# Kernel tuning notes

Measured on AMD Instinct MI355X. Metric: run time of the kernel, lower is better.

The kernel has to match this reference:

```python
import jax, jax.numpy as jnp
import numpy as np

B, N, D, L = 32, 1000, 256, 3


def setup_inputs() -> dict:
    key = jax.random.key(0)
    k1, k2, k3, k4 = jax.random.split(key, 4)
    x = jax.random.normal(k1, (B, N, D), dtype=jnp.float32)
    node_feature = jax.random.normal(k2, (B, N, D), dtype=jnp.float32)
    # GCNConv weights (PyG Linear, glorot) and biases, stacked over layers
    scale = jnp.sqrt(6.0 / (D + D)).astype(jnp.float32)
    Ws = jax.random.uniform(k3, (L, D, D), minval=-1.0, maxval=1.0, dtype=jnp.float32) * scale
    bs = jnp.zeros((L, D), dtype=jnp.float32)
    return {"x": x, "node_feature": node_feature, "Ws": Ws, "bs": bs}


def _gcn_norm_adj(n):
    # self_loop=False -> adjacency is all-ones (diagonal included), so
    # add_remaining_self_loops is a no-op; deg = n for every node.
    adj = jnp.ones((n, n), dtype=jnp.float32)
    deg = adj.sum(axis=1)
    dinv = jax.lax.rsqrt(deg)
    return dinv[:, None] * adj * dinv[None, :]  # == ones/n


def reference(x, node_feature, Ws, bs):
    # x is unused by the math (only its size is inspected in the original).
    A_norm = _gcn_norm_adj(node_feature.shape[1])
    h = node_feature
    for l in range(L):
        h = jnp.einsum('bnd,de->bne', h, Ws[l])          # linear transform
        h = jnp.einsum('mn,bnd->bmd', A_norm, h) + bs[l]  # normalized aggregation + bias
        if l < L - 1:
            h = jax.nn.relu(h)  # dropout is identity in eval mode
    update_node_feature = h + node_feature  # residual (unconditional in source)
    return (update_node_feature, node_feature)
```

## Files before the change

kernel.cpp:

```cpp
#include <hip/hip_runtime.h>

#define BB 32
#define NN 1000
#define DD 256
#define SS 25
#define RPS 40
#define ELEMS (BB * NN * DD)

__global__ __launch_bounds__(256) void k_colsum(const float* __restrict__ nf,
                                                float* __restrict__ partial) {
    const int s = blockIdx.x, b = blockIdx.y, t = threadIdx.x;
    const int rg = t >> 6, dg = t & 63;
    const float4* src = (const float4*)nf;
    float4 acc = make_float4(0.f, 0.f, 0.f, 0.f);
#pragma unroll
    for (int c = 0; c < RPS / 4; c++) {
        const int n = s * RPS + c * 4 + rg;
        float4 v = src[(b * NN + n) * (DD / 4) + dg];
        acc.x += v.x; acc.y += v.y; acc.z += v.z; acc.w += v.w;
    }
    __shared__ float red[1024];
    ((float4*)red)[rg * 64 + dg] = acc;
    __syncthreads();
    float sum = 0.f;
#pragma unroll
    for (int r = 0; r < 4; r++) sum += red[r * 256 + t];
    partial[(s * BB + b) * DD + t] = sum;
}

__global__ __launch_bounds__(256) void k_mlp(const float* __restrict__ partial,
                                             const float* __restrict__ Ws,
                                             const float* __restrict__ bsv,
                                             float* __restrict__ hrow) {
    const int b = blockIdx.x, t = threadIdx.x;
    __shared__ float h[DD];
    float sum = 0.f;
#pragma unroll 5
    for (int s = 0; s < SS; s++) sum += partial[(s * BB + b) * DD + t];
    h[t] = sum * (1.0f / (float)NN);
    __syncthreads();
    for (int l = 0; l < 3; l++) {
        const float* W = Ws + l * DD * DD;
        float acc = 0.f;
#pragma unroll 8
        for (int k4 = 0; k4 < DD / 4; k4++) {
            const float4 hv = ((const float4*)h)[k4];
            const int k = k4 * 4;
            acc += hv.x * W[(k + 0) * DD + t];
            acc += hv.y * W[(k + 1) * DD + t];
            acc += hv.z * W[(k + 2) * DD + t];
            acc += hv.w * W[(k + 3) * DD + t];
        }
        float o = acc + bsv[l * DD + t];
        if (l < 2) o = fmaxf(o, 0.f);
        __syncthreads();
        h[t] = o;
        __syncthreads();
    }
    hrow[b * DD + t] = h[t];
}

__global__ __launch_bounds__(256) void k_out(const float* __restrict__ nf,
                                             const float* __restrict__ hrow,
                                             float* __restrict__ out) {
    const int i = blockIdx.x * 256 + threadIdx.x;
    const int e = i * 4;
    const int b = e / (NN * DD);
    const int d0 = e & (DD - 1);
    float4 v = ((const float4*)nf)[i];
    float4 hv = *(const float4*)(hrow + b * DD + d0);
    float4 o = make_float4(v.x + hv.x, v.y + hv.y, v.z + hv.z, v.w + hv.w);
    ((float4*)out)[i] = o;
    ((float4*)(out + ELEMS))[i] = v;
}

extern "C" void kernel_launch(void* const* d_in, const int* in_sizes, int n_in,
                              void* d_out, int out_size, void* d_ws, size_t ws_size,
                              hipStream_t stream) {
    const float* nf  = (const float*)d_in[1];
    const float* Ws  = (const float*)d_in[2];
    const float* bsv = (const float*)d_in[3];
    float* out = (float*)d_out;

    float* partial = (float*)d_ws;
    float* hrow    = partial + SS * BB * DD;

    k_colsum<<<dim3(SS, BB), 256, 0, stream>>>(nf, partial);
    k_mlp<<<BB, 256, 0, stream>>>(partial, Ws, bsv, hrow);
    k_out<<<(ELEMS / 4) / 256, 256, 0, stream>>>(nf, hrow, out);
}
```

Baseline: 137.2 us.

## Fuse passthrough copy into column-sum pass and MLP into output pass

Replaces the three kernels with two. The first pass reads node features once, writes the passthrough copy and computes per-slice column sums. The second pass has each of 256 blocks recompute its batch's three-layer MLP on the mean and then write the residual output for its slice. This removes one launch and the hrow round trip, and the copy no longer needs its own read. The cost is 8x redundant MLP compute and only 256 blocks for the streaming passes, which may underfill the GPU.

```diff
diff --git a/kernel.cpp b/kernel.cpp
--- a/kernel.cpp
+++ b/kernel.cpp
@@ -3,41 +3,47 @@
 #define BB 32
 #define NN 1000
 #define DD 256
-#define SS 25
-#define RPS 40
 #define ELEMS (BB * NN * DD)
+#define SLICES 8
+#define ROWS 125
+#define F4S (ROWS * DD / 4)
 
-__global__ __launch_bounds__(256) void k_colsum(const float* __restrict__ nf,
-                                                float* __restrict__ partial) {
-    const int s = blockIdx.x, b = blockIdx.y, t = threadIdx.x;
-    const int rg = t >> 6, dg = t & 63;
+__global__ __launch_bounds__(256) void k_stage(const float* __restrict__ nf,
+                                               float* __restrict__ out1,
+                                               float* __restrict__ partial) {
+    const int j = blockIdx.x, t = threadIdx.x;
+    const int b = j >> 3, s = j & 7;
+    const int base = (b * NN + s * ROWS) * (DD / 4);
     const float4* src = (const float4*)nf;
+    float4* dst = (float4*)out1;
     float4 acc = make_float4(0.f, 0.f, 0.f, 0.f);
-#pragma unroll
-    for (int c = 0; c < RPS / 4; c++) {
-        const int n = s * RPS + c * 4 + rg;
-        float4 v = src[(b * NN + n) * (DD / 4) + dg];
+#pragma unroll 4
+    for (int idx = t; idx < F4S; idx += 256) {
+        float4 v = src[base + idx];
+        dst[base + idx] = v;
         acc.x += v.x; acc.y += v.y; acc.z += v.z; acc.w += v.w;
     }
     __shared__ float red[1024];
-    ((float4*)red)[rg * 64 + dg] = acc;
+    ((float4*)red)[(t >> 6) * 64 + (t & 63)] = acc;
     __syncthreads();
     float sum = 0.f;
 #pragma unroll
     for (int r = 0; r < 4; r++) sum += red[r * 256 + t];
-    partial[(s * BB + b) * DD + t] = sum;
+    partial[j * DD + t] = sum;
 }
 
-__global__ __launch_bounds__(256) void k_mlp(const float* __restrict__ partial,
-                                             const float* __restrict__ Ws,
-                                             const float* __restrict__ bsv,
-                                             float* __restrict__ hrow) {
-    const int b = blockIdx.x, t = threadIdx.x;
+__global__ __launch_bounds__(256) void k_mlp_out(const float* __restrict__ nf,
+                                                 const float* __restrict__ partial,
+                                                 const float* __restrict__ Ws,
+                                                 const float* __restrict__ bsv,
+                                                 float* __restrict__ out0) {
+    const int j = blockIdx.x, t = threadIdx.x;
+    const int b = j >> 3, s = j & 7;
     __shared__ float h[DD];
-    float sum = 0.f;
-#pragma unroll 5
-    for (int s = 0; s < SS; s++) sum += partial[(s * BB + b) * DD + t];
-    h[t] = sum * (1.0f / (float)NN);
+    float m = 0.f;
+#pragma unroll
+    for (int i = 0; i < SLICES; i++) m += partial[(b * SLICES + i) * DD + t];
+    h[t] = m * (1.0f / (float)NN);
     __syncthreads();
     for (int l = 0; l < 3; l++) {
         const float* W = Ws + l * DD * DD;
@@ -57,21 +63,15 @@
         h[t] = o;
         __syncthreads();
     }
-    hrow[b * DD + t] = h[t];
-}
-
-__global__ __launch_bounds__(256) void k_out(const float* __restrict__ nf,
-                                             const float* __restrict__ hrow,
-                                             float* __restrict__ out) {
-    const int i = blockIdx.x * 256 + threadIdx.x;
-    const int e = i * 4;
-    const int b = e / (NN * DD);
-    const int d0 = e & (DD - 1);
-    float4 v = ((const float4*)nf)[i];
-    float4 hv = *(const float4*)(hrow + b * DD + d0);
-    float4 o = make_float4(v.x + hv.x, v.y + hv.y, v.z + hv.z, v.w + hv.w);
-    ((float4*)out)[i] = o;
-    ((float4*)(out + ELEMS))[i] = v;
+    const int base = (b * NN + s * ROWS) * (DD / 4);
+    const float4 hv = ((const float4*)h)[t & 63];
+    const float4* src = (const float4*)nf;
+    float4* dst = (float4*)out0;
+#pragma unroll 4
+    for (int idx = t; idx < F4S; idx += 256) {
+        float4 v = src[base + idx];
+        dst[base + idx] = make_float4(v.x + hv.x, v.y + hv.y, v.z + hv.z, v.w + hv.w);
+    }
 }
 
 extern "C" void kernel_launch(void* const* d_in, const int* in_sizes, int n_in,
@@ -80,12 +80,11 @@
     const float* nf  = (const float*)d_in[1];
     const float* Ws  = (const float*)d_in[2];
     const float* bsv = (const float*)d_in[3];
-    float* out = (float*)d_out;
+    float* out0 = (float*)d_out;
+    float* out1 = out0 + ELEMS;
 
     float* partial = (float*)d_ws;
-    float* hrow    = partial + SS * BB * DD;
 
-    k_colsum<<<dim3(SS, BB), 256, 0, stream>>>(nf, partial);
-    k_mlp<<<BB, 256, 0, stream>>>(partial, Ws, bsv, hrow);
-    k_out<<<(ELEMS / 4) / 256, 256, 0, stream>>>(nf, hrow, out);
+    k_stage<<<BB * SLICES, 256, 0, stream>>>(nf, out1, partial);
+    k_mlp_out<<<BB * SLICES, 256, 0, stream>>>(nf, partial, Ws, bsv, out0);
 }
```

Measured after the change: 134.9 us. Within noise of the previous version (-1.7%).
